# Kernel optimization log

Hardware: AMD Instinct MI355X
Metric: run time of the kernel (lower is better)

## Reference

```python
import jax, jax.numpy as jnp
import numpy as np

N, D = 8192, 128
TEMPERATURE = 128.0


def setup_inputs() -> dict:
    key = jax.random.key(0)
    kx, ka = jax.random.split(key)
    x = jax.random.normal(kx, (N, D), dtype=jnp.float32)
    a = jax.random.normal(ka, (N, D), dtype=jnp.float32)
    return {"x": x, "a": a}


def reference(x, a):
    """uLSIF loss, 2D branch, exp_parameterization='inner_product', reduction='mean'.

    L_i = -2 * sim[i,i] + mean_{j != i} sim[i,j]^2,  sim = exp(x @ a.T / T)
    """
    n = x.shape[0]
    sim = jnp.exp(jnp.matmul(x, a.T) / TEMPERATURE)  # [N, N]
    sim_pos = jnp.diagonal(sim)                      # [N]
    # off-diagonal squared mean without a boolean-mask gather:
    # sum_j sim[i,j]^2 - sim[i,i]^2, divided by (N-1)
    row_sq_sum = jnp.sum(sim * sim, axis=1)          # [N]
    sim_neg_square = (row_sq_sum - sim_pos * sim_pos) / (n - 1)
    lora_loss = -2.0 * sim_pos + sim_neg_square      # [N]
    return jnp.mean(lora_loss)
```

## Files before the change

kernel.cpp:

```cpp
#include <hip/hip_runtime.h>


#define NN 8192
#define DD 128

typedef __attribute__((ext_vector_type(4))) float f32x4;
typedef __attribute__((ext_vector_type(8))) _Float16 f16x8;

__global__ void convert_kernel(const float4* __restrict__ x, const float4* __restrict__ a,
                               f16x8* __restrict__ xf, f16x8* __restrict__ af) {
    const float C2 = (float)(2.0 / (128.0 * 0.69314718055994530942));
    int j  = blockIdx.x * 256 + threadIdx.x;
    int m  = j >> 17;
    int jj = j & 131071;
    int f  = jj >> 6;
    int l  = jj & 63;
    int rg = f >> 2, ks = f & 3;
    int row = rg * 16 + (l & 15);
    int kf  = ks * 32 + (l >> 4) * 8;
    int base = row * 32 + (kf >> 2);
    const float4* in = m ? a : x;
    float4 v0 = in[base];
    float4 v1 = in[base + 1];
    float s = m ? C2 : 1.0f;
    f16x8 o;
    o[0] = (_Float16)(v0.x * s); o[1] = (_Float16)(v0.y * s);
    o[2] = (_Float16)(v0.z * s); o[3] = (_Float16)(v0.w * s);
    o[4] = (_Float16)(v1.x * s); o[5] = (_Float16)(v1.y * s);
    o[6] = (_Float16)(v1.z * s); o[7] = (_Float16)(v1.w * s);
    (m ? af : xf)[(size_t)f * 64 + l] = o;
}

__global__ void diag_kernel(const float4* __restrict__ x, const float4* __restrict__ a,
                            double* __restrict__ s1p, double* __restrict__ s3p) {
    int t = threadIdx.x;
    int row = blockIdx.x * 8 + (t >> 5);
    int c = t & 31;
    float4 xv = x[row * 32 + c];
    float4 av = a[row * 32 + c];
    float d = xv.x * av.x + xv.y * av.y + xv.z * av.z + xv.w * av.w;
#pragma unroll
    for (int off = 16; off > 0; off >>= 1) d += __shfl_down(d, off, 32);
    __shared__ double rr[8];
    if ((t & 31) == 0) rr[t >> 5] = exp((double)d * (1.0 / 128.0));
    __syncthreads();
    if (t == 0) {
        double s1 = 0.0, s3 = 0.0;
#pragma unroll
        for (int k = 0; k < 8; ++k) { s1 += rr[k]; s3 += rr[k] * rr[k]; }
        s1p[blockIdx.x] = s1;
        s3p[blockIdx.x] = s3;
    }
}

__global__ __launch_bounds__(512, 2) void gemm_exp_sum(const f16x8* __restrict__ xf,
                                                       const f16x8* __restrict__ af,
                                                       double* __restrict__ s2p) {
    const int tid  = threadIdx.x;
    const int lane = tid & 63;
    const int wid  = tid >> 6;
    const int bm    = blockIdx.x >> 3;
    const int chunk = blockIdx.x & 7;
    const int wm = wid >> 1;
    const int wn = wid & 1;

    const int fA0 = (bm * 16 + wm * 4) * 4;
    f16x8 afr[4][4];
#pragma unroll
    for (int mi = 0; mi < 4; ++mi)
#pragma unroll
        for (int ks = 0; ks < 4; ++ks)
            afr[mi][ks] = xf[(size_t)(fA0 + mi * 4 + ks) * 64 + lane];

    const int fB0 = (chunk * 64 + wn * 4) * 4;
    f16x8 bfr[3][4];
#pragma unroll
    for (int kk = 0; kk < 3; ++kk)
#pragma unroll
        for (int ni = 0; ni < 4; ++ni)
            bfr[kk][ni] = af[(size_t)(fB0 + ni * 4 + kk) * 64 + lane];

    f32x4 acc[4][4];
#pragma unroll
    for (int mi = 0; mi < 4; ++mi)
#pragma unroll
        for (int ni = 0; ni < 4; ++ni) acc[mi][ni] = f32x4{0.f, 0.f, 0.f, 0.f};
    float ls0 = 0.f, ls1 = 0.f, ls2 = 0.f, ls3 = 0.f;

#pragma unroll
    for (int kk = 0; kk < 32; ++kk) {
        const int ks = kk & 3;
        const int sl = kk % 3;
#pragma unroll
        for (int mi = 0; mi < 4; ++mi)
#pragma unroll
            for (int ni = 0; ni < 4; ++ni)
                acc[mi][ni] = __builtin_amdgcn_mfma_f32_16x16x32_f16(
                    afr[mi][ks], bfr[sl][ni], acc[mi][ni], 0, 0, 0);
        if (kk + 3 < 32) {
            const int kn = kk + 3, tn = kn >> 2, ksn = kn & 3;
#pragma unroll
            for (int ni = 0; ni < 4; ++ni)
                bfr[sl][ni] = af[(size_t)(fB0 + tn * 32 + ni * 4 + ksn) * 64 + lane];
        }
        if (ks == 3) {
#pragma unroll
            for (int mi = 0; mi < 4; ++mi)
#pragma unroll
                for (int ni = 0; ni < 4; ++ni) {
                    ls0 += __builtin_amdgcn_exp2f(acc[mi][ni][0]);
                    ls1 += __builtin_amdgcn_exp2f(acc[mi][ni][1]);
                    ls2 += __builtin_amdgcn_exp2f(acc[mi][ni][2]);
                    ls3 += __builtin_amdgcn_exp2f(acc[mi][ni][3]);
                    acc[mi][ni] = f32x4{0.f, 0.f, 0.f, 0.f};
                }
        }
    }

    float lsum = (ls0 + ls1) + (ls2 + ls3);
#pragma unroll
    for (int off = 32; off > 0; off >>= 1) lsum += __shfl_down(lsum, off);

    __shared__ double wred[8];
    if (lane == 0) wred[wid] = (double)lsum;
    __syncthreads();
    if (tid == 0) {
        double s = 0.0;
#pragma unroll
        for (int k = 0; k < 8; ++k) s += wred[k];
        s2p[blockIdx.x] = s;
    }
}

__global__ void finalize_kernel(const double* __restrict__ s1p, const double* __restrict__ s3p,
                                const double* __restrict__ s2p, float* __restrict__ out) {
    int t = threadIdx.x;
    double v1 = s1p[t];
    double v3 = s3p[t];
    double v2 = (t < 256) ? s2p[t] : 0.0;
#pragma unroll
    for (int off = 32; off > 0; off >>= 1) {
        v1 += __shfl_down(v1, off);
        v3 += __shfl_down(v3, off);
        v2 += __shfl_down(v2, off);
    }
    __shared__ double r1[16], r2[16], r3[16];
    int wid = t >> 6, lane = t & 63;
    if (lane == 0) { r1[wid] = v1; r2[wid] = v2; r3[wid] = v3; }
    __syncthreads();
    if (t == 0) {
        double S1 = 0.0, S2 = 0.0, S3 = 0.0;
#pragma unroll
        for (int k = 0; k < 16; ++k) { S1 += r1[k]; S2 += r2[k]; S3 += r3[k]; }
        double res = (-2.0 * S1 + (S2 - S3) / (double)(NN - 1)) / (double)NN;
        out[0] = (float)res;
    }
}

extern "C" void kernel_launch(void* const* d_in, const int* in_sizes, int n_in,
                              void* d_out, int out_size, void* d_ws, size_t ws_size,
                              hipStream_t stream) {
    const float* x = (const float*)d_in[0];
    const float* a = (const float*)d_in[1];
    float* out = (float*)d_out;
    char* ws = (char*)d_ws;

    double* s1p = (double*)ws;
    double* s3p = (double*)(ws + 8192);
    double* s2p = (double*)(ws + 16384);
    f16x8*  xf  = (f16x8*)(ws + 32768);
    f16x8*  af  = (f16x8*)(ws + 32768 + (size_t)NN * DD * 2);

    convert_kernel<<<1024, 256, 0, stream>>>((const float4*)x, (const float4*)a, xf, af);
    diag_kernel<<<1024, 256, 0, stream>>>((const float4*)x, (const float4*)a, s1p, s3p);
    gemm_exp_sum<<<256, 512, 0, stream>>>(xf, af, s2p);
    finalize_kernel<<<1, 1024, 0, stream>>>(s1p, s3p, s2p, out);
}
```

Measured before the change: 85.30 us.

## Fuse conversion with diagonal kernel and double-buffer B fragments in GEMM

Merges the fp16 conversion/swizzle kernel and the diagonal exp kernel into one launch that reads x and a once and writes both swizzled fp16 buffers plus diagonal partial sums. The GEMM inner loop changes from a 3-slot rolling prefetch over a 4x4 warp tile to a two-buffer ping-pong over a 4x2 tile. Accumulators are now reset and exponentiated per 32-column step in a non-unrolled loop. This removes one launch and a redundant read of the inputs, and lowers register pressure, but each warp now does fewer MFMAs per B fragment load.

```diff
diff --git a/kernel.cpp b/kernel.cpp
--- a/kernel.cpp
+++ b/kernel.cpp
@@ -7,40 +7,37 @@
 typedef __attribute__((ext_vector_type(4))) float f32x4;
 typedef __attribute__((ext_vector_type(8))) _Float16 f16x8;
 
-__global__ void convert_kernel(const float4* __restrict__ x, const float4* __restrict__ a,
-                               f16x8* __restrict__ xf, f16x8* __restrict__ af) {
+__global__ void conv_diag_kernel(const float4* __restrict__ x, const float4* __restrict__ a,
+                                 char* __restrict__ xf, char* __restrict__ af,
+                                 double* __restrict__ s1p, double* __restrict__ s3p) {
     const float C2 = (float)(2.0 / (128.0 * 0.69314718055994530942));
-    int j  = blockIdx.x * 256 + threadIdx.x;
-    int m  = j >> 17;
-    int jj = j & 131071;
-    int f  = jj >> 6;
-    int l  = jj & 63;
-    int rg = f >> 2, ks = f & 3;
-    int row = rg * 16 + (l & 15);
-    int kf  = ks * 32 + (l >> 4) * 8;
-    int base = row * 32 + (kf >> 2);
-    const float4* in = m ? a : x;
-    float4 v0 = in[base];
-    float4 v1 = in[base + 1];
-    float s = m ? C2 : 1.0f;
-    f16x8 o;
-    o[0] = (_Float16)(v0.x * s); o[1] = (_Float16)(v0.y * s);
-    o[2] = (_Float16)(v0.z * s); o[3] = (_Float16)(v0.w * s);
-    o[4] = (_Float16)(v1.x * s); o[5] = (_Float16)(v1.y * s);
-    o[6] = (_Float16)(v1.z * s); o[7] = (_Float16)(v1.w * s);
-    (m ? af : xf)[(size_t)f * 64 + l] = o;
-}
+    int t = threadIdx.x;
+    int i = blockIdx.x * 256 + t;
+    int row = i >> 5;
+    int q   = i & 31;
+    int ks  = q >> 3;
+    int l   = (((q & 7) >> 1) << 4) | (row & 15);
+    int f   = (row >> 4) * 4 + ks;
+    size_t off = (size_t)f * 1024 + (size_t)l * 16 + (size_t)(i & 1) * 8;
 
-__global__ void diag_kernel(const float4* __restrict__ x, const float4* __restrict__ a,
-                            double* __restrict__ s1p, double* __restrict__ s3p) {
-    int t = threadIdx.x;
-    int row = blockIdx.x * 8 + (t >> 5);
-    int c = t & 31;
-    float4 xv = x[row * 32 + c];
-    float4 av = a[row * 32 + c];
+    float4 xv = x[i];
+    float4 av = a[i];
+    ushort4 xu, au;
+    xu.x = __builtin_bit_cast(unsigned short, (_Float16)xv.x);
+    xu.y = __builtin_bit_cast(unsigned short, (_Float16)xv.y);
+    xu.z = __builtin_bit_cast(unsigned short, (_Float16)xv.z);
+    xu.w = __builtin_bit_cast(unsigned short, (_Float16)xv.w);
+    au.x = __builtin_bit_cast(unsigned short, (_Float16)(av.x * C2));
+    au.y = __builtin_bit_cast(unsigned short, (_Float16)(av.y * C2));
+    au.z = __builtin_bit_cast(unsigned short, (_Float16)(av.z * C2));
+    au.w = __builtin_bit_cast(unsigned short, (_Float16)(av.w * C2));
+    *(ushort4*)(xf + off) = xu;
+    *(ushort4*)(af + off) = au;
+
     float d = xv.x * av.x + xv.y * av.y + xv.z * av.z + xv.w * av.w;
 #pragma unroll
-    for (int off = 16; off > 0; off >>= 1) d += __shfl_down(d, off, 32);
+    for (int o = 16; o > 0; o >>= 1) d += __shfl_down(d, o, 32);
+
     __shared__ double rr[8];
     if ((t & 31) == 0) rr[t >> 5] = exp((double)d * (1.0 / 128.0));
     __syncthreads();
@@ -72,54 +69,58 @@
         for (int ks = 0; ks < 4; ++ks)
             afr[mi][ks] = xf[(size_t)(fA0 + mi * 4 + ks) * 64 + lane];
 
-    const int fB0 = (chunk * 64 + wn * 4) * 4;
-    f16x8 bfr[3][4];
+    const int fB0 = (chunk * 64 + wn * 2) * 4;
+
+    f16x8 b0[2][4], b1[2][4];
 #pragma unroll
-    for (int kk = 0; kk < 3; ++kk)
+    for (int ni = 0; ni < 2; ++ni)
 #pragma unroll
-        for (int ni = 0; ni < 4; ++ni)
-            bfr[kk][ni] = af[(size_t)(fB0 + ni * 4 + kk) * 64 + lane];
+        for (int ks = 0; ks < 4; ++ks)
+            b0[ni][ks] = af[(size_t)(fB0 + ni * 4 + ks) * 64 + lane];
 
-    f32x4 acc[4][4];
-#pragma unroll
-    for (int mi = 0; mi < 4; ++mi)
-#pragma unroll
-        for (int ni = 0; ni < 4; ++ni) acc[mi][ni] = f32x4{0.f, 0.f, 0.f, 0.f};
+    f32x4 acc[4][2];
     float ls0 = 0.f, ls1 = 0.f, ls2 = 0.f, ls3 = 0.f;
 
-#pragma unroll
-    for (int kk = 0; kk < 32; ++kk) {
-        const int ks = kk & 3;
-        const int sl = kk % 3;
-#pragma unroll
-        for (int mi = 0; mi < 4; ++mi)
-#pragma unroll
-            for (int ni = 0; ni < 4; ++ni)
-                acc[mi][ni] = __builtin_amdgcn_mfma_f32_16x16x32_f16(
-                    afr[mi][ks], bfr[sl][ni], acc[mi][ni], 0, 0, 0);
-        if (kk + 3 < 32) {
-            const int kn = kk + 3, tn = kn >> 2, ksn = kn & 3;
-#pragma unroll
-            for (int ni = 0; ni < 4; ++ni)
-                bfr[sl][ni] = af[(size_t)(fB0 + tn * 32 + ni * 4 + ksn) * 64 + lane];
-        }
-        if (ks == 3) {
-#pragma unroll
-            for (int mi = 0; mi < 4; ++mi)
-#pragma unroll
-                for (int ni = 0; ni < 4; ++ni) {
-                    ls0 += __builtin_amdgcn_exp2f(acc[mi][ni][0]);
-                    ls1 += __builtin_amdgcn_exp2f(acc[mi][ni][1]);
-                    ls2 += __builtin_amdgcn_exp2f(acc[mi][ni][2]);
-                    ls3 += __builtin_amdgcn_exp2f(acc[mi][ni][3]);
-                    acc[mi][ni] = f32x4{0.f, 0.f, 0.f, 0.f};
-                }
-        }
+#define PREFETCH(B, S)                                                              \
+    {                                                                               \
+        const int sc = (S) > 15 ? 15 : (S);                                         \
+        _Pragma("unroll") for (int ni = 0; ni < 2; ++ni)                            \
+            _Pragma("unroll") for (int ks = 0; ks < 4; ++ks)                        \
+                B[ni][ks] = af[(size_t)(fB0 + sc * 16 + ni * 4 + ks) * 64 + lane];  \
     }
+
+#define COMPUTE(B)                                                                  \
+    {                                                                               \
+        _Pragma("unroll") for (int mi = 0; mi < 4; ++mi)                            \
+            _Pragma("unroll") for (int ni = 0; ni < 2; ++ni)                        \
+                acc[mi][ni] = f32x4{0.f, 0.f, 0.f, 0.f};                            \
+        _Pragma("unroll") for (int ks = 0; ks < 4; ++ks)                            \
+            _Pragma("unroll") for (int mi = 0; mi < 4; ++mi)                        \
+                _Pragma("unroll") for (int ni = 0; ni < 2; ++ni)                    \
+                    acc[mi][ni] = __builtin_amdgcn_mfma_f32_16x16x32_f16(           \
+                        afr[mi][ks], B[ni][ks], acc[mi][ni], 0, 0, 0);              \
+        _Pragma("unroll") for (int mi = 0; mi < 4; ++mi)                            \
+            _Pragma("unroll") for (int ni = 0; ni < 2; ++ni) {                      \
+                ls0 += __builtin_amdgcn_exp2f(acc[mi][ni][0]);                      \
+                ls1 += __builtin_amdgcn_exp2f(acc[mi][ni][1]);                      \
+                ls2 += __builtin_amdgcn_exp2f(acc[mi][ni][2]);                      \
+                ls3 += __builtin_amdgcn_exp2f(acc[mi][ni][3]);                      \
+            }                                                                       \
+    }
+
+#pragma unroll 1
+    for (int s = 0; s < 16; s += 2) {
+        PREFETCH(b1, s + 1);
+        COMPUTE(b0);
+        PREFETCH(b0, s + 2);
+        COMPUTE(b1);
+    }
+#undef PREFETCH
+#undef COMPUTE
 
     float lsum = (ls0 + ls1) + (ls2 + ls3);
 #pragma unroll
-    for (int off = 32; off > 0; off >>= 1) lsum += __shfl_down(lsum, off);
+    for (int o = 32; o > 0; o >>= 1) lsum += __shfl_down(lsum, o);
 
     __shared__ double wred[8];
     if (lane == 0) wred[wid] = (double)lsum;
@@ -139,10 +140,10 @@
     double v3 = s3p[t];
     double v2 = (t < 256) ? s2p[t] : 0.0;
 #pragma unroll
-    for (int off = 32; off > 0; off >>= 1) {
-        v1 += __shfl_down(v1, off);
-        v3 += __shfl_down(v3, off);
-        v2 += __shfl_down(v2, off);
+    for (int o = 32; o > 0; o >>= 1) {
+        v1 += __shfl_down(v1, o);
+        v3 += __shfl_down(v3, o);
+        v2 += __shfl_down(v2, o);
     }
     __shared__ double r1[16], r2[16], r3[16];
     int wid = t >> 6, lane = t & 63;
@@ -168,11 +169,11 @@
     double* s1p = (double*)ws;
     double* s3p = (double*)(ws + 8192);
     double* s2p = (double*)(ws + 16384);
-    f16x8*  xf  = (f16x8*)(ws + 32768);
-    f16x8*  af  = (f16x8*)(ws + 32768 + (size_t)NN * DD * 2);
+    char*   xf  = ws + 32768;
+    char*   af  = ws + 32768 + (size_t)NN * DD * 2;
 
-    convert_kernel<<<1024, 256, 0, stream>>>((const float4*)x, (const float4*)a, xf, af);
-    diag_kernel<<<1024, 256, 0, stream>>>((const float4*)x, (const float4*)a, s1p, s3p);
-    gemm_exp_sum<<<256, 512, 0, stream>>>(xf, af, s2p);
+    conv_diag_kernel<<<1024, 256, 0, stream>>>((const float4*)x, (const float4*)a,
+                                               xf, af, s1p, s3p);
+    gemm_exp_sum<<<256, 512, 0, stream>>>((const f16x8*)xf, (const f16x8*)af, s2p);
     finalize_kernel<<<1, 1024, 0, stream>>>(s1p, s3p, s2p, out);
 }
```

After: 102.2 us. 19.8% more time.
